# Performance work log

Hardware: AMD Instinct MI355X
Metric: run time of the kernel (lower is better)

The kernel has to match this reference:

```python
import jax, jax.numpy as jnp
import numpy as np

N, D, H, Y = 2048, 768, 12, 64


def setup_inputs() -> dict:
    key = jax.random.key(0)
    kg, kq, kk = jax.random.split(key, 3)
    g = jax.random.normal(kg, (N, D), dtype=jnp.float32)
    Wq = jax.random.normal(kq, (H, Y, D), dtype=jnp.float32)
    Wk = jax.random.normal(kk, (H, Y, D), dtype=jnp.float32)
    return {"g": g, "Wq": Wq, "Wk": Wk}


def reference(g, Wq, Wk):
    # g: [N, D]; Wq, Wk: [H, Y, D]
    beta = 1.0 / jnp.sqrt(jnp.asarray(Y, dtype=g.dtype))
    K = jnp.einsum('kd,hzd->khz', g, Wk)          # [N, H, Y]
    Q = jnp.einsum('qd,hzd->qhz', g, Wq)          # [N, H, Y]
    scores = beta * jnp.einsum('qhz,khz->hqk', Q, K)  # [H, N, N]
    A = jax.nn.logsumexp(scores, axis=-1)         # [H, N]
    return (-1.0 / beta) * A.sum()
```

## Files before the change

kernel.cpp:

```cpp
#include <hip/hip_runtime.h>
#include <hip/hip_bf16.h>

#define NN 2048
#define DD 768
#define HH 12
#define HW 1536
#define G_ELEMS (NN*DD)
#define W1_ELEMS (HH*64*DD)
#define SPLITS 4
#define KPW (NN/SPLITS)
#define NCH (KPW/64)

typedef __attribute__((ext_vector_type(8))) short bf16x8;
typedef __attribute__((ext_vector_type(4))) float f32x4;

__device__ __forceinline__ float exp2g(float x) { return __builtin_amdgcn_exp2f(x); }
__device__ __forceinline__ float log2g(float x) { return __builtin_amdgcn_logf(x); }

#define QSCALE 0.18033688011112042f
__global__ __launch_bounds__(256) void convert_kernel(
    const float* __restrict__ g, const float* __restrict__ Wq,
    const float* __restrict__ Wk, __hip_bfloat16* __restrict__ gB,
    __hip_bfloat16* __restrict__ wB, float* __restrict__ out) {
  if (blockIdx.x == 0 && threadIdx.x == 0) out[0] = 0.0f;
  int base = (blockIdx.x * 256 + threadIdx.x) * 4;
  float4 v;
  __hip_bfloat16* dst;
  if (base < G_ELEMS) {
    v = *reinterpret_cast<const float4*>(g + base);
    dst = gB + base;
  } else if (base < G_ELEMS + W1_ELEMS) {
    int o = base - G_ELEMS;
    v = *reinterpret_cast<const float4*>(Wq + o);
    v.x *= QSCALE; v.y *= QSCALE; v.z *= QSCALE; v.w *= QSCALE;
    dst = wB + o;
  } else {
    int o = base - (G_ELEMS + W1_ELEMS);
    v = *reinterpret_cast<const float4*>(Wk + o);
    dst = wB + W1_ELEMS + o;
  }
  __hip_bfloat16 h0 = __float2bfloat16(v.x), h1 = __float2bfloat16(v.y);
  __hip_bfloat16 h2 = __float2bfloat16(v.z), h3 = __float2bfloat16(v.w);
  ushort4 u;
  u.x = *reinterpret_cast<unsigned short*>(&h0);
  u.y = *reinterpret_cast<unsigned short*>(&h1);
  u.z = *reinterpret_cast<unsigned short*>(&h2);
  u.w = *reinterpret_cast<unsigned short*>(&h3);
  *reinterpret_cast<ushort4*>(dst) = u;
}

#define LDP 72
__global__ __launch_bounds__(256) void proj_kernel(
    const __hip_bfloat16* __restrict__ gB, const __hip_bfloat16* __restrict__ wB,
    __hip_bfloat16* __restrict__ QK) {
  __shared__ __align__(16) __hip_bfloat16 As[2][64 * LDP];
  __shared__ __align__(16) __hip_bfloat16 Bs[2][64 * LDP];
  const int t = threadIdx.x;
  const int wave = t >> 6, lane = t & 63;
  const int lr = lane & 15, lg = lane >> 4;
  const int wm = wave & 1, wn = wave >> 1;
  const int bm = blockIdx.x, bn = blockIdx.y;
  const int r0 = t >> 3, s0 = (t & 7) * 8;
  const int r1 = (t + 256) >> 3, s1 = s0;

  f32x4 acc[2][2] = {};

  {
    *reinterpret_cast<uint4*>(&As[0][r0 * LDP + s0]) =
        *reinterpret_cast<const uint4*>(gB + (bm * 64 + r0) * DD + s0);
    *reinterpret_cast<uint4*>(&As[0][r1 * LDP + s1]) =
        *reinterpret_cast<const uint4*>(gB + (bm * 64 + r1) * DD + s1);
    *reinterpret_cast<uint4*>(&Bs[0][r0 * LDP + s0]) =
        *reinterpret_cast<const uint4*>(wB + (bn * 64 + r0) * DD + s0);
    *reinterpret_cast<uint4*>(&Bs[0][r1 * LDP + s1]) =
        *reinterpret_cast<const uint4*>(wB + (bn * 64 + r1) * DD + s1);
  }
  __syncthreads();

  for (int it = 0; it < 12; ++it) {
    const int cur = it & 1;
    uint4 na0, na1, nb0, nb1;
    if (it < 11) {
      int kt = (it + 1) * 64;
      na0 = *reinterpret_cast<const uint4*>(gB + (bm * 64 + r0) * DD + kt + s0);
      na1 = *reinterpret_cast<const uint4*>(gB + (bm * 64 + r1) * DD + kt + s1);
      nb0 = *reinterpret_cast<const uint4*>(wB + (bn * 64 + r0) * DD + kt + s0);
      nb1 = *reinterpret_cast<const uint4*>(wB + (bn * 64 + r1) * DD + kt + s1);
    }
#pragma unroll
    for (int ks = 0; ks < 2; ++ks) {
      bf16x8 a[2], b[2];
#pragma unroll
      for (int mt = 0; mt < 2; ++mt)
        a[mt] = *reinterpret_cast<const bf16x8*>(&As[cur][(wm * 32 + mt * 16 + lr) * LDP + ks * 32 + lg * 8]);
#pragma unroll
      for (int nt = 0; nt < 2; ++nt)
        b[nt] = *reinterpret_cast<const bf16x8*>(&Bs[cur][(wn * 32 + nt * 16 + lr) * LDP + ks * 32 + lg * 8]);
#pragma unroll
      for (int mt = 0; mt < 2; ++mt)
#pragma unroll
        for (int nt = 0; nt < 2; ++nt)
          acc[mt][nt] = __builtin_amdgcn_mfma_f32_16x16x32_bf16(a[mt], b[nt], acc[mt][nt], 0, 0, 0);
    }
    if (it < 11) {
      *reinterpret_cast<uint4*>(&As[cur ^ 1][r0 * LDP + s0]) = na0;
      *reinterpret_cast<uint4*>(&As[cur ^ 1][r1 * LDP + s1]) = na1;
      *reinterpret_cast<uint4*>(&Bs[cur ^ 1][r0 * LDP + s0]) = nb0;
      *reinterpret_cast<uint4*>(&Bs[cur ^ 1][r1 * LDP + s1]) = nb1;
      __syncthreads();
    }
  }
#pragma unroll
  for (int mt = 0; mt < 2; ++mt) {
    int row = bm * 64 + wm * 32 + mt * 16 + lg * 4;
#pragma unroll
    for (int nt = 0; nt < 2; ++nt) {
      int col = bn * 64 + wn * 32 + nt * 16 + lr;
#pragma unroll
      for (int r = 0; r < 4; ++r)
        QK[(row + r) * HW + col] = __float2bfloat16(acc[mt][nt][r]);
    }
  }
}

#define LDA 72
__global__ __launch_bounds__(256) void attn_kernel(
    const __hip_bfloat16* __restrict__ QK, float2* __restrict__ part) {
  __shared__ __align__(16) __hip_bfloat16 Ks[2][64 * LDA];
  const int t = threadIdx.x;
  const int wave = t >> 6, lane = t & 63;
  const int lr = lane & 15, lg = lane >> 4;
  const int q0 = blockIdx.x * 128, h = blockIdx.y, sp = blockIdx.z;
  const int k0 = sp * KPW;
  const int r0 = t >> 3, s0 = (t & 7) * 8;
  const int r1 = (t + 256) >> 3, s1 = s0;
  const int colK = DD + h * 64;

  bf16x8 aq[2][2];
#pragma unroll
  for (int mt = 0; mt < 2; ++mt)
#pragma unroll
    for (int z = 0; z < 2; ++z)
      aq[mt][z] = *reinterpret_cast<const bf16x8*>(
          QK + (q0 + wave * 32 + mt * 16 + lr) * HW + h * 64 + z * 32 + lg * 8);

  *reinterpret_cast<uint4*>(&Ks[0][r0 * LDA + s0]) =
      *reinterpret_cast<const uint4*>(QK + (k0 + r0) * HW + colK + s0);
  *reinterpret_cast<uint4*>(&Ks[0][r1 * LDA + s1]) =
      *reinterpret_cast<const uint4*>(QK + (k0 + r1) * HW + colK + s1);
  __syncthreads();

  float m[2][4], l[2][4];
#pragma unroll
  for (int mt = 0; mt < 2; ++mt)
#pragma unroll
    for (int r = 0; r < 4; ++r) { m[mt][r] = -3.0e38f; l[mt][r] = 0.0f; }

  for (int ci = 0; ci < NCH; ++ci) {
    const int cur = ci & 1;
    uint4 n0, n1;
    if (ci < NCH - 1) {
      int kc = k0 + (ci + 1) * 64;
      n0 = *reinterpret_cast<const uint4*>(QK + (kc + r0) * HW + colK + s0);
      n1 = *reinterpret_cast<const uint4*>(QK + (kc + r1) * HW + colK + s1);
    }
    bf16x8 b[4][2];
#pragma unroll
    for (int nt = 0; nt < 4; ++nt)
#pragma unroll
      for (int z = 0; z < 2; ++z)
        b[nt][z] = *reinterpret_cast<const bf16x8*>(&Ks[cur][(nt * 16 + lr) * LDA + z * 32 + lg * 8]);

    f32x4 s[2][4] = {};
#pragma unroll
    for (int mt = 0; mt < 2; ++mt)
#pragma unroll
      for (int nt = 0; nt < 4; ++nt)
#pragma unroll
        for (int z = 0; z < 2; ++z)
          s[mt][nt] = __builtin_amdgcn_mfma_f32_16x16x32_bf16(aq[mt][z], b[nt][z], s[mt][nt], 0, 0, 0);

#pragma unroll
    for (int mt = 0; mt < 2; ++mt)
#pragma unroll
      for (int r = 0; r < 4; ++r) {
        float v0 = s[mt][0][r], v1 = s[mt][1][r], v2 = s[mt][2][r], v3 = s[mt][3][r];
        float cm = fmaxf(fmaxf(v0, v1), fmaxf(v2, v3));
        float mn = fmaxf(m[mt][r], cm);
        float p = exp2g(v0 - mn) + exp2g(v1 - mn) +
                  exp2g(v2 - mn) + exp2g(v3 - mn);
        l[mt][r] = l[mt][r] * exp2g(m[mt][r] - mn) + p;
        m[mt][r] = mn;
      }
    if (ci < NCH - 1) {
      *reinterpret_cast<uint4*>(&Ks[cur ^ 1][r0 * LDA + s0]) = n0;
      *reinterpret_cast<uint4*>(&Ks[cur ^ 1][r1 * LDA + s1]) = n1;
      __syncthreads();
    }
  }
#pragma unroll
  for (int msk = 1; msk <= 8; msk <<= 1) {
#pragma unroll
    for (int mt = 0; mt < 2; ++mt)
#pragma unroll
      for (int r = 0; r < 4; ++r) {
        float mo = __shfl_xor(m[mt][r], msk);
        float lo = __shfl_xor(l[mt][r], msk);
        float mn = fmaxf(m[mt][r], mo);
        l[mt][r] = l[mt][r] * exp2g(m[mt][r] - mn) + lo * exp2g(mo - mn);
        m[mt][r] = mn;
      }
  }
  if (lr == 0) {
#pragma unroll
    for (int mt = 0; mt < 2; ++mt)
#pragma unroll
      for (int r = 0; r < 4; ++r) {
        int q = q0 + wave * 32 + mt * 16 + lg * 4 + r;
        part[(sp * HH + h) * NN + q] = make_float2(m[mt][r], l[mt][r]);
      }
  }
}

__global__ __launch_bounds__(1024) void reduce_kernel(
    const float2* __restrict__ part, float* __restrict__ out) {
  const int t = threadIdx.x;
  const int row = blockIdx.x * 1024 + t;
  float2 p0 = part[row];
  float2 p1 = part[24576 + row];
  float2 p2 = part[49152 + row];
  float2 p3 = part[73728 + row];
  float mm = fmaxf(fmaxf(p0.x, p1.x), fmaxf(p2.x, p3.x));
  float ll = p0.y * exp2g(p0.x - mm) + p1.y * exp2g(p1.x - mm) +
             p2.y * exp2g(p2.x - mm) + p3.y * exp2g(p3.x - mm);
  float lse = mm + log2g(ll);
#pragma unroll
  for (int msk = 1; msk <= 32; msk <<= 1)
    lse += __shfl_xor(lse, msk);
  __shared__ float wsum[16];
  if ((t & 63) == 0) wsum[t >> 6] = lse;
  __syncthreads();
  if (t == 0) {
    float s = 0.0f;
#pragma unroll
    for (int i = 0; i < 16; ++i) s += wsum[i];
    atomicAdd(out, -5.545177444479562f * s);
  }
}

extern "C" void kernel_launch(void* const* d_in, const int* in_sizes, int n_in,
                              void* d_out, int out_size, void* d_ws, size_t ws_size,
                              hipStream_t stream) {
  const float* g  = (const float*)d_in[0];
  const float* Wq = (const float*)d_in[1];
  const float* Wk = (const float*)d_in[2];
  float* out = (float*)d_out;

  __hip_bfloat16* gB = (__hip_bfloat16*)d_ws;
  __hip_bfloat16* wB = gB + G_ELEMS;
  __hip_bfloat16* QK = wB + 2 * W1_ELEMS;
  float2* part = (float2*)gB;

  convert_kernel<<<2688, 256, 0, stream>>>(g, Wq, Wk, gB, wB, out);
  proj_kernel<<<dim3(32, 24), 256, 0, stream>>>(gB, wB, QK);
  attn_kernel<<<dim3(16, HH, SPLITS), 256, 0, stream>>>(QK, part);
  reduce_kernel<<<24, 1024, 0, stream>>>(part, out);
}
```

Baseline: 96.10 us.

## Fuse fp32-to-bf16 conversion into projection GEMM and load K directly to registers

Removes the separate conversion kernel: the projection GEMM now reads fp32 g/Wq/Wk, applies the Q scale and converts to bf16 while staging tiles into shared memory. The attention kernel drops its shared-memory K staging and barriers, prefetching K fragments straight from global memory into registers, with a launch-bounds occupancy hint. This removes a kernel launch and a round trip of bf16 copies. In exchange the GEMM reads twice the bytes per tile and converts each tile repeatedly across blocks, and K loads are no longer shared across waves.

```diff
diff --git a/kernel.cpp b/kernel.cpp
--- a/kernel.cpp
+++ b/kernel.cpp
@@ -5,8 +5,6 @@
 #define DD 768
 #define HH 12
 #define HW 1536
-#define G_ELEMS (NN*DD)
-#define W1_ELEMS (HH*64*DD)
 #define SPLITS 4
 #define KPW (NN/SPLITS)
 #define NCH (KPW/64)
@@ -18,74 +16,77 @@
 __device__ __forceinline__ float log2g(float x) { return __builtin_amdgcn_logf(x); }
 
 #define QSCALE 0.18033688011112042f
-__global__ __launch_bounds__(256) void convert_kernel(
-    const float* __restrict__ g, const float* __restrict__ Wq,
-    const float* __restrict__ Wk, __hip_bfloat16* __restrict__ gB,
-    __hip_bfloat16* __restrict__ wB, float* __restrict__ out) {
-  if (blockIdx.x == 0 && threadIdx.x == 0) out[0] = 0.0f;
-  int base = (blockIdx.x * 256 + threadIdx.x) * 4;
-  float4 v;
-  __hip_bfloat16* dst;
-  if (base < G_ELEMS) {
-    v = *reinterpret_cast<const float4*>(g + base);
-    dst = gB + base;
-  } else if (base < G_ELEMS + W1_ELEMS) {
-    int o = base - G_ELEMS;
-    v = *reinterpret_cast<const float4*>(Wq + o);
-    v.x *= QSCALE; v.y *= QSCALE; v.z *= QSCALE; v.w *= QSCALE;
-    dst = wB + o;
-  } else {
-    int o = base - (G_ELEMS + W1_ELEMS);
-    v = *reinterpret_cast<const float4*>(Wk + o);
-    dst = wB + W1_ELEMS + o;
-  }
-  __hip_bfloat16 h0 = __float2bfloat16(v.x), h1 = __float2bfloat16(v.y);
-  __hip_bfloat16 h2 = __float2bfloat16(v.z), h3 = __float2bfloat16(v.w);
-  ushort4 u;
-  u.x = *reinterpret_cast<unsigned short*>(&h0);
-  u.y = *reinterpret_cast<unsigned short*>(&h1);
-  u.z = *reinterpret_cast<unsigned short*>(&h2);
-  u.w = *reinterpret_cast<unsigned short*>(&h3);
-  *reinterpret_cast<ushort4*>(dst) = u;
+
+__device__ __forceinline__ unsigned short bfbits(float x) {
+  __hip_bfloat16 h = __float2bfloat16(x);
+  return *reinterpret_cast<unsigned short*>(&h);
+}
+
+__device__ __forceinline__ void cvt_store(__hip_bfloat16* dst, float4 a, float4 b, float sc) {
+  union { uint4 v; unsigned short s[8]; } u;
+  u.s[0] = bfbits(a.x * sc); u.s[1] = bfbits(a.y * sc);
+  u.s[2] = bfbits(a.z * sc); u.s[3] = bfbits(a.w * sc);
+  u.s[4] = bfbits(b.x * sc); u.s[5] = bfbits(b.y * sc);
+  u.s[6] = bfbits(b.z * sc); u.s[7] = bfbits(b.w * sc);
+  *reinterpret_cast<uint4*>(dst) = u.v;
 }
 
 #define LDP 72
 __global__ __launch_bounds__(256) void proj_kernel(
-    const __hip_bfloat16* __restrict__ gB, const __hip_bfloat16* __restrict__ wB,
-    __hip_bfloat16* __restrict__ QK) {
+    const float* __restrict__ g, const float* __restrict__ Wq,
+    const float* __restrict__ Wk, __hip_bfloat16* __restrict__ QK,
+    float* __restrict__ out) {
   __shared__ __align__(16) __hip_bfloat16 As[2][64 * LDP];
   __shared__ __align__(16) __hip_bfloat16 Bs[2][64 * LDP];
+  if (blockIdx.x == 0 && blockIdx.y == 0 && threadIdx.x == 0) out[0] = 0.0f;
   const int t = threadIdx.x;
   const int wave = t >> 6, lane = t & 63;
   const int lr = lane & 15, lg = lane >> 4;
   const int wm = wave & 1, wn = wave >> 1;
   const int bm = blockIdx.x, bn = blockIdx.y;
   const int r0 = t >> 3, s0 = (t & 7) * 8;
-  const int r1 = (t + 256) >> 3, s1 = s0;
+  const int r1 = (t + 256) >> 3;
+
+  const float bscale = (bn < HH) ? QSCALE : 1.0f;
+  const float* wsrc = (bn < HH) ? Wq : Wk;
+  const int wrow = (bn < HH) ? bn * 64 : (bn - HH) * 64;
+
+  const float* ga0 = g + (bm * 64 + r0) * DD + s0;
+  const float* ga1 = g + (bm * 64 + r1) * DD + s0;
+  const float* gb0 = wsrc + (wrow + r0) * DD + s0;
+  const float* gb1 = wsrc + (wrow + r1) * DD + s0;
 
   f32x4 acc[2][2] = {};
 
   {
-    *reinterpret_cast<uint4*>(&As[0][r0 * LDP + s0]) =
-        *reinterpret_cast<const uint4*>(gB + (bm * 64 + r0) * DD + s0);
-    *reinterpret_cast<uint4*>(&As[0][r1 * LDP + s1]) =
-        *reinterpret_cast<const uint4*>(gB + (bm * 64 + r1) * DD + s1);
-    *reinterpret_cast<uint4*>(&Bs[0][r0 * LDP + s0]) =
-        *reinterpret_cast<const uint4*>(wB + (bn * 64 + r0) * DD + s0);
-    *reinterpret_cast<uint4*>(&Bs[0][r1 * LDP + s1]) =
-        *reinterpret_cast<const uint4*>(wB + (bn * 64 + r1) * DD + s1);
+    float4 a0 = *reinterpret_cast<const float4*>(ga0);
+    float4 a0h = *reinterpret_cast<const float4*>(ga0 + 4);
+    float4 a1 = *reinterpret_cast<const float4*>(ga1);
+    float4 a1h = *reinterpret_cast<const float4*>(ga1 + 4);
+    float4 b0 = *reinterpret_cast<const float4*>(gb0);
+    float4 b0h = *reinterpret_cast<const float4*>(gb0 + 4);
+    float4 b1 = *reinterpret_cast<const float4*>(gb1);
+    float4 b1h = *reinterpret_cast<const float4*>(gb1 + 4);
+    cvt_store(&As[0][r0 * LDP + s0], a0, a0h, 1.0f);
+    cvt_store(&As[0][r1 * LDP + s0], a1, a1h, 1.0f);
+    cvt_store(&Bs[0][r0 * LDP + s0], b0, b0h, bscale);
+    cvt_store(&Bs[0][r1 * LDP + s0], b1, b1h, bscale);
   }
   __syncthreads();
 
   for (int it = 0; it < 12; ++it) {
     const int cur = it & 1;
-    uint4 na0, na1, nb0, nb1;
+    float4 na0, na0h, na1, na1h, nb0, nb0h, nb1, nb1h;
     if (it < 11) {
-      int kt = (it + 1) * 64;
-      na0 = *reinterpret_cast<const uint4*>(gB + (bm * 64 + r0) * DD + kt + s0);
-      na1 = *reinterpret_cast<const uint4*>(gB + (bm * 64 + r1) * DD + kt + s1);
-      nb0 = *reinterpret_cast<const uint4*>(wB + (bn * 64 + r0) * DD + kt + s0);
-      nb1 = *reinterpret_cast<const uint4*>(wB + (bn * 64 + r1) * DD + kt + s1);
+      const int kt = (it + 1) * 64;
+      na0 = *reinterpret_cast<const float4*>(ga0 + kt);
+      na0h = *reinterpret_cast<const float4*>(ga0 + kt + 4);
+      na1 = *reinterpret_cast<const float4*>(ga1 + kt);
+      na1h = *reinterpret_cast<const float4*>(ga1 + kt + 4);
+      nb0 = *reinterpret_cast<const float4*>(gb0 + kt);
+      nb0h = *reinterpret_cast<const float4*>(gb0 + kt + 4);
+      nb1 = *reinterpret_cast<const float4*>(gb1 + kt);
+      nb1h = *reinterpret_cast<const float4*>(gb1 + kt + 4);
     }
 #pragma unroll
     for (int ks = 0; ks < 2; ++ks) {
@@ -103,10 +104,10 @@
           acc[mt][nt] = __builtin_amdgcn_mfma_f32_16x16x32_bf16(a[mt], b[nt], acc[mt][nt], 0, 0, 0);
     }
     if (it < 11) {
-      *reinterpret_cast<uint4*>(&As[cur ^ 1][r0 * LDP + s0]) = na0;
-      *reinterpret_cast<uint4*>(&As[cur ^ 1][r1 * LDP + s1]) = na1;
-      *reinterpret_cast<uint4*>(&Bs[cur ^ 1][r0 * LDP + s0]) = nb0;
-      *reinterpret_cast<uint4*>(&Bs[cur ^ 1][r1 * LDP + s1]) = nb1;
+      cvt_store(&As[cur ^ 1][r0 * LDP + s0], na0, na0h, 1.0f);
+      cvt_store(&As[cur ^ 1][r1 * LDP + s0], na1, na1h, 1.0f);
+      cvt_store(&Bs[cur ^ 1][r0 * LDP + s0], nb0, nb0h, bscale);
+      cvt_store(&Bs[cur ^ 1][r1 * LDP + s0], nb1, nb1h, bscale);
       __syncthreads();
     }
   }
@@ -123,18 +124,13 @@
   }
 }
 
-#define LDA 72
-__global__ __launch_bounds__(256) void attn_kernel(
+__global__ __launch_bounds__(256, 3) void attn_kernel(
     const __hip_bfloat16* __restrict__ QK, float2* __restrict__ part) {
-  __shared__ __align__(16) __hip_bfloat16 Ks[2][64 * LDA];
   const int t = threadIdx.x;
   const int wave = t >> 6, lane = t & 63;
   const int lr = lane & 15, lg = lane >> 4;
   const int q0 = blockIdx.x * 128, h = blockIdx.y, sp = blockIdx.z;
   const int k0 = sp * KPW;
-  const int r0 = t >> 3, s0 = (t & 7) * 8;
-  const int r1 = (t + 256) >> 3, s1 = s0;
-  const int colK = DD + h * 64;
 
   bf16x8 aq[2][2];
 #pragma unroll
@@ -144,11 +140,7 @@
       aq[mt][z] = *reinterpret_cast<const bf16x8*>(
           QK + (q0 + wave * 32 + mt * 16 + lr) * HW + h * 64 + z * 32 + lg * 8);
 
-  *reinterpret_cast<uint4*>(&Ks[0][r0 * LDA + s0]) =
-      *reinterpret_cast<const uint4*>(QK + (k0 + r0) * HW + colK + s0);
-  *reinterpret_cast<uint4*>(&Ks[0][r1 * LDA + s1]) =
-      *reinterpret_cast<const uint4*>(QK + (k0 + r1) * HW + colK + s1);
-  __syncthreads();
+  const __hip_bfloat16* kb = QK + (k0 + lr) * HW + DD + h * 64 + lg * 8;
 
   float m[2][4], l[2][4];
 #pragma unroll
@@ -156,20 +148,24 @@
 #pragma unroll
     for (int r = 0; r < 4; ++r) { m[mt][r] = -3.0e38f; l[mt][r] = 0.0f; }
 
+  bf16x8 b[4][2];
+#pragma unroll
+  for (int nt = 0; nt < 4; ++nt)
+#pragma unroll
+    for (int z = 0; z < 2; ++z)
+      b[nt][z] = *reinterpret_cast<const bf16x8*>(kb + nt * 16 * HW + z * 32);
+
+#pragma unroll
   for (int ci = 0; ci < NCH; ++ci) {
-    const int cur = ci & 1;
-    uint4 n0, n1;
+    bf16x8 nb[4][2];
     if (ci < NCH - 1) {
-      int kc = k0 + (ci + 1) * 64;
-      n0 = *reinterpret_cast<const uint4*>(QK + (kc + r0) * HW + colK + s0);
-      n1 = *reinterpret_cast<const uint4*>(QK + (kc + r1) * HW + colK + s1);
-    }
-    bf16x8 b[4][2];
-#pragma unroll
-    for (int nt = 0; nt < 4; ++nt)
-#pragma unroll
-      for (int z = 0; z < 2; ++z)
-        b[nt][z] = *reinterpret_cast<const bf16x8*>(&Ks[cur][(nt * 16 + lr) * LDA + z * 32 + lg * 8]);
+      const __hip_bfloat16* nk = kb + (ci + 1) * 64 * HW;
+#pragma unroll
+      for (int nt = 0; nt < 4; ++nt)
+#pragma unroll
+        for (int z = 0; z < 2; ++z)
+          nb[nt][z] = *reinterpret_cast<const bf16x8*>(nk + nt * 16 * HW + z * 32);
+    }
 
     f32x4 s[2][4] = {};
 #pragma unroll
@@ -192,12 +188,16 @@
         l[mt][r] = l[mt][r] * exp2g(m[mt][r] - mn) + p;
         m[mt][r] = mn;
       }
+
     if (ci < NCH - 1) {
-      *reinterpret_cast<uint4*>(&Ks[cur ^ 1][r0 * LDA + s0]) = n0;
-      *reinterpret_cast<uint4*>(&Ks[cur ^ 1][r1 * LDA + s1]) = n1;
-      __syncthreads();
-    }
-  }
+#pragma unroll
+      for (int nt = 0; nt < 4; ++nt)
+#pragma unroll
+        for (int z = 0; z < 2; ++z)
+          b[nt][z] = nb[nt][z];
+    }
+  }
+
 #pragma unroll
   for (int msk = 1; msk <= 8; msk <<= 1) {
 #pragma unroll
@@ -256,13 +256,10 @@
   const float* Wk = (const float*)d_in[2];
   float* out = (float*)d_out;
 
-  __hip_bfloat16* gB = (__hip_bfloat16*)d_ws;
-  __hip_bfloat16* wB = gB + G_ELEMS;
-  __hip_bfloat16* QK = wB + 2 * W1_ELEMS;
-  float2* part = (float2*)gB;
-
-  convert_kernel<<<2688, 256, 0, stream>>>(g, Wq, Wk, gB, wB, out);
-  proj_kernel<<<dim3(32, 24), 256, 0, stream>>>(gB, wB, QK);
+  __hip_bfloat16* QK = (__hip_bfloat16*)d_ws;
+  float2* part = (float2*)((char*)d_ws + (size_t)NN * HW * 2);
+
+  proj_kernel<<<dim3(32, 24), 256, 0, stream>>>(g, Wq, Wk, QK, out);
   attn_kernel<<<dim3(16, HH, SPLITS), 256, 0, stream>>>(QK, part);
   reduce_kernel<<<24, 1024, 0, stream>>>(part, out);
 }
```

New measurement: 106.8 us. 11.2% more time.
